# Performance work log

Hardware: AMD Instinct MI355X
Metric: run time of the kernel (lower is better)

Reference implementation:

```python
import jax, jax.numpy as jnp
import numpy as np

B, H, W, C = 16, 56, 56, 512
HEADS, WIN = 16, 7
HID = 2048
EPS = 1e-5


def _rel_pos_index(win):
    coords = np.stack(np.meshgrid(np.arange(win), np.arange(win), indexing='ij'))  # 2,w,w
    cf = coords.reshape(2, -1)  # 2, w*w
    rel = (cf[:, :, None] - cf[:, None, :]).transpose(1, 2, 0).astype(np.int64)  # N,N,2
    rel[..., 0] += win - 1
    rel[..., 1] += win - 1
    rel[..., 0] *= 2 * win - 1
    return jnp.asarray(rel.sum(-1))  # N,N


def setup_inputs() -> dict:
    key = jax.random.key(0)
    ks = jax.random.split(key, 12)
    s = 0.02
    return {
        'x': jax.random.normal(ks[0], (B, H * W, C), jnp.float32),
        'norm1_w': jnp.ones((C,), jnp.float32),
        'norm1_b': jnp.zeros((C,), jnp.float32),
        'qkv_w': jax.random.normal(ks[1], (3 * C, C), jnp.float32) * s,
        'qkv_b': jnp.zeros((3 * C,), jnp.float32),
        'proj_w': jax.random.normal(ks[2], (C, C), jnp.float32) * s,
        'proj_b': jnp.zeros((C,), jnp.float32),
        'rel_bias_table': jax.random.normal(ks[3], ((2 * WIN - 1) ** 2, HEADS), jnp.float32) * s,
        'norm2_w': jnp.ones((C,), jnp.float32),
        'norm2_b': jnp.zeros((C,), jnp.float32),
        'fc1_w': jax.random.normal(ks[4], (HID, C), jnp.float32) * s,
        'fc1_b': jnp.zeros((HID,), jnp.float32),
        'fc2_w': jax.random.normal(ks[5], (C, HID), jnp.float32) * s,
        'fc2_b': jnp.zeros((C,), jnp.float32),
        'rel_pos_index': _rel_pos_index(WIN),
    }


def _ln(x, w, b):
    m = jnp.mean(x, -1, keepdims=True)
    v = jnp.mean((x - m) ** 2, -1, keepdims=True)
    return (x - m) * jax.lax.rsqrt(v + EPS) * w + b


def reference(x, norm1_w, norm1_b, qkv_w, qkv_b, proj_w, proj_b, rel_bias_table,
              norm2_w, norm2_b, fc1_w, fc1_b, fc2_w, fc2_b, rel_pos_index):
    N = WIN * WIN
    hd = C // HEADS
    shortcut = x
    h = _ln(x, norm1_w, norm1_b).reshape(B, H, W, C)
    # window partition -> (nW*B, N, C)
    h = h.reshape(B, H // WIN, WIN, W // WIN, WIN, C).transpose(0, 1, 3, 2, 4, 5)
    xw = h.reshape(-1, N, C)
    Bw = xw.shape[0]
    qkv = (xw @ qkv_w.T + qkv_b).reshape(Bw, N, 3, HEADS, hd).transpose(2, 0, 3, 1, 4)
    q, k, v = qkv[0], qkv[1], qkv[2]  # (Bw, heads, N, hd)
    q = q * (hd ** -0.5)
    attn = jnp.einsum('bhnd,bhmd->bhnm', q, k)
    bias = rel_bias_table[rel_pos_index.reshape(-1)].reshape(N, N, HEADS).transpose(2, 0, 1)
    attn = jax.nn.softmax(attn + bias[None], axis=-1)
    out = jnp.einsum('bhnm,bhmd->bhnd', attn, v).transpose(0, 2, 1, 3).reshape(Bw, N, C)
    out = out @ proj_w.T + proj_b
    # window reverse -> (B, H*W, C)
    out = out.reshape(B, H // WIN, W // WIN, WIN, WIN, C).transpose(0, 1, 3, 2, 4, 5)
    out = out.reshape(B, H * W, C)
    x = shortcut + out
    h2 = _ln(x, norm2_w, norm2_b)
    h2 = jax.nn.gelu(h2 @ fc1_w.T + fc1_b, approximate=False) @ fc2_w.T + fc2_b
    return x + h2
```

## Files before the change

kernel.cpp:

```cpp
#include <hip/hip_runtime.h>
#include <stdint.h>

#define B_    16
#define C_    512
#define HEADS 16
#define NTOK  49
#define ROWS  (16*56*56)

typedef __attribute__((ext_vector_type(8))) __bf16 bf16x8;
typedef __attribute__((ext_vector_type(4))) float  f32x4;
typedef __attribute__((ext_vector_type(8))) unsigned short u16x8;
typedef __attribute__((ext_vector_type(4))) unsigned short u16x4;

__device__ __forceinline__ unsigned short f2bf(float f) {
  union { float f; uint32_t u; } x; x.f = f;
  uint32_t r = x.u + 0x7FFFu + ((x.u >> 16) & 1u);
  return (unsigned short)(r >> 16);
}
__device__ __forceinline__ float bf2f(unsigned short u) {
  union { uint32_t u; float f; } x; x.u = ((uint32_t)u) << 16;
  return x.f;
}

template<int EPI>
__global__ __launch_bounds__(512, 2)
void gemm_bt(const unsigned short* __restrict__ A,
             const unsigned short* __restrict__ Bt,
             const float* __restrict__ bias,
             const float* __restrict__ res,
             void* __restrict__ outp,
             int N, int K, int ldb, int nbn)
{
  __shared__ __align__(16) unsigned short As[2][256*64];
  __shared__ __align__(16) unsigned short Bs[2][256*64];

  const int nwg = gridDim.x;
  const int q8 = nwg >> 3, r8 = nwg & 7;
  const int xcd = blockIdx.x & 7, ixc = blockIdx.x >> 3;
  const int l = (xcd < r8 ? xcd * (q8 + 1) : r8 * (q8 + 1) + (xcd - r8) * q8) + ixc;
  const int bm = l / nbn, bn = l % nbn;

  const int tid  = threadIdx.x;
  const int wave = tid >> 6;
  const int lane = tid & 63;
  const int wr = wave >> 2, wc = wave & 3;

  const unsigned short* Ag = A  + (size_t)bm * 256 * K;
  const unsigned short* Bg = Bt + (size_t)bn * 256 * ldb;

  f32x4 acc[8][4] = {};
  const int fr = lane & 15;
  const int kq = lane >> 4;
  const int sx = fr & 7;

  auto STAGE = [&](int buf, int t) {
    const int k0 = t << 6;
    #pragma unroll
    for (int li = 0; li < 4; ++li) {
      const int slot = tid + li * 512;
      const int r = slot >> 3;
      const int g = (slot & 7) ^ (r & 7);
      __builtin_amdgcn_global_load_lds(
        (const __attribute__((address_space(1))) void*)(Ag + (size_t)r * K + k0 + g * 8),
        (__attribute__((address_space(3))) void*)(&As[buf][(li * 512 + wave * 64) * 8]), 16, 0, 0);
    }
    #pragma unroll
    for (int li = 0; li < 4; ++li) {
      const int slot = tid + li * 512;
      const int r = slot >> 3;
      const int g = (slot & 7) ^ (r & 7);
      __builtin_amdgcn_global_load_lds(
        (const __attribute__((address_space(1))) void*)(Bg + (size_t)r * ldb + k0 + g * 8),
        (__attribute__((address_space(3))) void*)(&Bs[buf][(li * 512 + wave * 64) * 8]), 16, 0, 0);
    }
  };

  const int nt = K >> 6;
  STAGE(0, 0);
  for (int t = 0; t < nt; ++t) {
    const int c = t & 1;
    if (t + 1 < nt) {
      STAGE(c ^ 1, t + 1);
      asm volatile("s_waitcnt vmcnt(8)" ::: "memory");
    } else {
      asm volatile("s_waitcnt vmcnt(0)" ::: "memory");
    }
    __builtin_amdgcn_s_barrier();

    #pragma unroll
    for (int ks = 0; ks < 2; ++ks) {
      bf16x8 a[8], b[4];
      #pragma unroll
      for (int m = 0; m < 8; ++m)
        a[m] = *(const bf16x8*)&As[c][(wr * 128 + m * 16 + fr) * 64
                                      + (((ks * 4 + kq) ^ sx) * 8)];
      #pragma unroll
      for (int n = 0; n < 4; ++n)
        b[n] = *(const bf16x8*)&Bs[c][(wc * 64 + n * 16 + fr) * 64
                                      + (((ks * 4 + kq) ^ sx) * 8)];
      __builtin_amdgcn_s_setprio(1);
      #pragma unroll
      for (int m = 0; m < 8; ++m)
        #pragma unroll
        for (int n = 0; n < 4; ++n)
          acc[m][n] = __builtin_amdgcn_mfma_f32_16x16x32_bf16(a[m], b[n], acc[m][n], 0, 0, 0);
      __builtin_amdgcn_s_setprio(0);
    }

    asm volatile("s_waitcnt lgkmcnt(0)" ::: "memory");
    __builtin_amdgcn_s_barrier();
  }

  const int rq = lane >> 4;
  #pragma unroll
  for (int m = 0; m < 8; ++m) {
    #pragma unroll
    for (int n = 0; n < 4; ++n) {
      const int gcol = bn * 256 + wc * 64 + n * 16 + fr;
      const float bv = (EPI == 3) ? 0.f : bias[gcol];
      #pragma unroll
      for (int r = 0; r < 4; ++r) {
        const int grow = bm * 256 + wr * 128 + m * 16 + rq * 4 + r;
        const size_t off = (size_t)grow * N + gcol;
        float v = acc[m][n][r] + bv;
        if (EPI == 0) {
          ((unsigned short*)outp)[off] = f2bf(v);
        } else if (EPI == 1) {
          v = 0.5f * v * (1.0f + erff(v * 0.70710678118654752f));
          ((unsigned short*)outp)[off] = f2bf(v);
        } else {
          ((float*)outp)[off] = v + res[off];
        }
      }
    }
  }
}

__global__ __launch_bounds__(256)
void ln_bf16(const float* __restrict__ x, const float* __restrict__ w,
             const float* __restrict__ b, unsigned short* __restrict__ out)
{
  const int row  = blockIdx.x * 4 + (threadIdx.x >> 6);
  const int lane = threadIdx.x & 63;
  const float4* xr = (const float4*)(x + (size_t)row * C_);
  const float4 u = xr[lane * 2];
  const float4 v = xr[lane * 2 + 1];
  const float vals[8] = {u.x,u.y,u.z,u.w,v.x,v.y,v.z,v.w};
  float s = 0.f, s2 = 0.f;
  #pragma unroll
  for (int j = 0; j < 8; ++j) { s += vals[j]; s2 += vals[j]*vals[j]; }
  #pragma unroll
  for (int off = 1; off < 64; off <<= 1) {
    s  += __shfl_xor(s,  off);
    s2 += __shfl_xor(s2, off);
  }
  const float mean = s * (1.0f/512.0f);
  const float rstd = rsqrtf(s2 * (1.0f/512.0f) - mean*mean + 1e-5f);
  u16x8 o;
  #pragma unroll
  for (int j = 0; j < 8; ++j) {
    const int col = lane * 8 + j;
    o[j] = f2bf((vals[j] - mean) * rstd * w[col] + b[col]);
  }
  *(u16x8*)&out[(size_t)row * C_ + lane * 8] = o;
}

__global__ __launch_bounds__(512)
void attn_win2(const unsigned short* __restrict__ qkv,
               const unsigned short* __restrict__ biasBf,
               unsigned short* __restrict__ outb, int i0)
{
  __shared__ float  Ksh[8][NTOK*32];
  __shared__ float  Vsh[8][NTOK*32];
  __shared__ unsigned short Bsh[8][NTOK*NTOK];
  const int bi   = blockIdx.x;
  const int half = bi & 1, winl = bi >> 1;
  const int bbl = winl >> 6, wy = (winl >> 3) & 7, wx = winl & 7;
  const int wave = threadIdx.x >> 6, lane = threadIdx.x & 63;
  const int head = half * 8 + wave;

  for (int i = lane; i < NTOK*NTOK; i += 64)
    Bsh[wave][i] = biasBf[head * (NTOK*NTOK) + i];

  float q[32];
  size_t gl = 0, gg = 0;
  if (lane < NTOK) {
    const int r = lane / 7, c = lane % 7;
    gl = (size_t)bbl * 3136 + (size_t)((wy*7 + r) * 56 + (wx*7 + c));
    gg = gl + (size_t)i0 * 3136;
    const unsigned short* qp = qkv + gl * 1536 + head * 32;
    #pragma unroll
    for (int d = 0; d < 32; d += 4) {
      const u16x4 qv = *(const u16x4*)&qp[d];
      const u16x4 kv = *(const u16x4*)&qp[512 + d];
      const u16x4 vv = *(const u16x4*)&qp[1024 + d];
      #pragma unroll
      for (int e = 0; e < 4; ++e) {
        q[d+e] = bf2f(qv[e]);
        Ksh[wave][lane*32 + d + e] = bf2f(kv[e]);
        Vsh[wave][lane*32 + d + e] = bf2f(vv[e]);
      }
    }
  }
  if (lane < NTOK) {
    float s[NTOK];
    float mx = -1e30f;
    for (int j = 0; j < NTOK; ++j) {
      float dot = 0.f;
      #pragma unroll
      for (int d = 0; d < 32; ++d) dot += q[d] * Ksh[wave][j*32 + d];
      const float val = dot * 0.17677669529663687f
                      + bf2f(Bsh[wave][lane*NTOK + j]);
      s[j] = val;
      mx = fmaxf(mx, val);
    }
    float sum = 0.f;
    for (int j = 0; j < NTOK; ++j) { s[j] = __expf(s[j] - mx); sum += s[j]; }
    const float inv = 1.0f / sum;
    float o[32];
    #pragma unroll
    for (int d = 0; d < 32; ++d) o[d] = 0.f;
    for (int j = 0; j < NTOK; ++j) {
      const float p = s[j] * inv;
      #pragma unroll
      for (int d = 0; d < 32; ++d) o[d] += p * Vsh[wave][j*32 + d];
    }
    unsigned short* op = outb + gg * 512 + head * 32;
    #pragma unroll
    for (int d = 0; d < 32; d += 4) {
      u16x4 ov;
      #pragma unroll
      for (int e = 0; e < 4; ++e) ov[e] = f2bf(o[d+e]);
      *(u16x4*)&op[d] = ov;
    }
  }
}

__global__ void build_bias(const float* __restrict__ table, const int* __restrict__ idx,
                           unsigned short* __restrict__ biasBf)
{
  const int i = blockIdx.x * 256 + threadIdx.x;
  if (i >= HEADS * NTOK * NTOK) return;
  const int h  = i / (NTOK*NTOK);
  const int ij = i - h * (NTOK*NTOK);
  biasBf[i] = f2bf(table[idx[ij] * HEADS + h]);
}

__global__ void conv_bf16(const float* __restrict__ in, unsigned short* __restrict__ out, int n4)
{
  const int i = blockIdx.x * 256 + threadIdx.x;
  if (i >= n4) return;
  const float4 v = ((const float4*)in)[i];
  u16x4 o; o[0]=f2bf(v.x); o[1]=f2bf(v.y); o[2]=f2bf(v.z); o[3]=f2bf(v.w);
  ((u16x4*)out)[i] = o;
}

extern "C" void kernel_launch(void* const* d_in, const int* in_sizes, int n_in,
                              void* d_out, int out_size, void* d_ws, size_t ws_size,
                              hipStream_t stream)
{
  const float* x     = (const float*)d_in[0];
  const float* n1w   = (const float*)d_in[1];
  const float* n1b   = (const float*)d_in[2];
  const float* qkvw  = (const float*)d_in[3];
  const float* qkvb  = (const float*)d_in[4];
  const float* projw = (const float*)d_in[5];
  const float* projb = (const float*)d_in[6];
  const float* rbt   = (const float*)d_in[7];
  const float* n2w   = (const float*)d_in[8];
  const float* n2b   = (const float*)d_in[9];
  const float* fc1w  = (const float*)d_in[10];
  const float* fc1b  = (const float*)d_in[11];
  const float* fc2w  = (const float*)d_in[12];
  const float* fc2b  = (const float*)d_in[13];
  const int*   rpi   = (const int*)d_in[14];
  float* out = (float*)d_out;

  char* p = (char*)d_ws;
  auto alloc = [&](size_t bytes) -> char* {
    char* q = p; p += (bytes + 255) & ~(size_t)255; return q;
  };
  unsigned short* wqB  = (unsigned short*)alloc((size_t)1536 * 512 * 2);
  unsigned short* wpB  = (unsigned short*)alloc((size_t)512  * 512 * 2);
  unsigned short* w1B  = (unsigned short*)alloc((size_t)2048 * 512 * 2);
  unsigned short* w2B  = (unsigned short*)alloc((size_t)512  * 2048 * 2);
  unsigned short* biasBf = (unsigned short*)alloc((size_t)HEADS * NTOK * NTOK * 2);
  unsigned short* bufX = (unsigned short*)alloc((size_t)ROWS * 512 * 2);
  const size_t used = (size_t)(p - (char*)d_ws);
  const size_t Rbytes = (ws_size > used) ? ws_size - used : 0;
  unsigned short* R = (unsigned short*)p;

  int ic = 0;
  for (int c = 16; c >= 4; c >>= 1)
    if ((size_t)c * 3136 * 1536 * 2 <= Rbytes) { ic = c; break; }
  int hc = 0;
  for (int c = 2048; c >= 256; c >>= 1)
    if ((size_t)ROWS * c * 2 <= Rbytes) { hc = c; break; }
  if (ic == 0 || hc == 0) return;

  conv_bf16<<<(1536*512/4 + 255)/256, 256, 0, stream>>>(qkvw, wqB, 1536*512/4);
  conv_bf16<<<(512*512/4  + 255)/256, 256, 0, stream>>>(projw, wpB, 512*512/4);
  conv_bf16<<<(2048*512/4 + 255)/256, 256, 0, stream>>>(fc1w, w1B, 2048*512/4);
  conv_bf16<<<(512*2048/4 + 255)/256, 256, 0, stream>>>(fc2w, w2B, 512*2048/4);
  build_bias<<<(HEADS*NTOK*NTOK + 255)/256, 256, 0, stream>>>(rbt, rpi, biasBf);

  ln_bf16<<<ROWS/4, 256, 0, stream>>>(x, n1w, n1b, bufX);

  for (int i0 = 0; i0 < B_; i0 += ic) {
    const int nbm = ic * 3136 / 256, nbn = 6;
    gemm_bt<0><<<nbm * nbn, 512, 0, stream>>>(
        bufX + (size_t)i0*3136*512, wqB, qkvb, nullptr, R, 1536, 512, 512, nbn);
    attn_win2<<<ic*64*2, 512, 0, stream>>>(R, biasBf, bufX, i0);
  }

  gemm_bt<2><<<(ROWS/256) * 2, 512, 0, stream>>>(
      bufX, wpB, projb, x, out, 512, 512, 512, 2);

  ln_bf16<<<ROWS/4, 256, 0, stream>>>(out, n2w, n2b, bufX);

  for (int h0 = 0; h0 < 2048; h0 += hc) {
    gemm_bt<1><<<(ROWS/256) * (hc/256), 512, 0, stream>>>(
        bufX, w1B + (size_t)h0*512, fc1b + h0, nullptr, R, hc, 512, 512, hc/256);
    if (h0 == 0)
      gemm_bt<2><<<(ROWS/256) * 2, 512, 0, stream>>>(
          R, w2B + h0, fc2b, out, out, 512, hc, 2048, 2);
    else
      gemm_bt<3><<<(ROWS/256) * 2, 512, 0, stream>>>(
          R, w2B + h0, nullptr, out, out, 512, hc, 2048, 2);
  }
}
```

Measured before the change: 861.4 us.

## Use 4-stage 32-wide K pipeline in GEMM and tanh-approx GELU

Restructures the GEMM main loop from a double-buffered BK=64 scheme into a four-deep ring of BK=32 stages, with three stages of loads in flight and an adjusted LDS swizzle. The goal is to hide more global memory latency behind MFMA work with the same LDS footprint, at the cost of a barrier pair per 32-wide K step. It also replaces the exact erf GELU with a tanh-form approximation built on a sigmoid and fast exp. That is cheaper per element but departs from the reference's exact GELU (approximate=False).

```diff
diff --git a/kernel.cpp b/kernel.cpp
--- a/kernel.cpp
+++ b/kernel.cpp
@@ -11,6 +11,9 @@
 typedef __attribute__((ext_vector_type(4))) float  f32x4;
 typedef __attribute__((ext_vector_type(8))) unsigned short u16x8;
 typedef __attribute__((ext_vector_type(4))) unsigned short u16x4;
+
+#define AS1 __attribute__((address_space(1)))
+#define AS3 __attribute__((address_space(3)))
 
 __device__ __forceinline__ unsigned short f2bf(float f) {
   union { float f; uint32_t u; } x; x.f = f;
@@ -31,8 +34,8 @@
              void* __restrict__ outp,
              int N, int K, int ldb, int nbn)
 {
-  __shared__ __align__(16) unsigned short As[2][256*64];
-  __shared__ __align__(16) unsigned short Bs[2][256*64];
+  __shared__ __align__(16) unsigned short As[4 * 8192];
+  __shared__ __align__(16) unsigned short Bs[4 * 8192];
 
   const int nwg = gridDim.x;
   const int q8 = nwg >> 3, r8 = nwg & 7;
@@ -51,64 +54,67 @@
   f32x4 acc[8][4] = {};
   const int fr = lane & 15;
   const int kq = lane >> 4;
-  const int sx = fr & 7;
-
-  auto STAGE = [&](int buf, int t) {
-    const int k0 = t << 6;
-    #pragma unroll
-    for (int li = 0; li < 4; ++li) {
-      const int slot = tid + li * 512;
-      const int r = slot >> 3;
-      const int g = (slot & 7) ^ (r & 7);
+  const int kxor = kq ^ (fr & 3);
+
+  auto STAGE = [&](int s) {
+    const int r = s & 3;
+    const int k0 = s << 5;
+    #pragma unroll
+    for (int i = 0; i < 2; ++i) {
+      const int u = tid + i * 512;
+      const int row = u >> 2;
+      const int gs = (u & 3) ^ (row & 3);
       __builtin_amdgcn_global_load_lds(
-        (const __attribute__((address_space(1))) void*)(Ag + (size_t)r * K + k0 + g * 8),
-        (__attribute__((address_space(3))) void*)(&As[buf][(li * 512 + wave * 64) * 8]), 16, 0, 0);
-    }
-    #pragma unroll
-    for (int li = 0; li < 4; ++li) {
-      const int slot = tid + li * 512;
-      const int r = slot >> 3;
-      const int g = (slot & 7) ^ (r & 7);
+        (const AS1 void*)(Ag + (size_t)row * K + k0 + gs * 8),
+        (AS3 void*)(&As[r * 8192 + (wave * 64 + i * 512) * 8]), 16, 0, 0);
+    }
+    #pragma unroll
+    for (int i = 0; i < 2; ++i) {
+      const int u = tid + i * 512;
+      const int row = u >> 2;
+      const int gs = (u & 3) ^ (row & 3);
       __builtin_amdgcn_global_load_lds(
-        (const __attribute__((address_space(1))) void*)(Bg + (size_t)r * ldb + k0 + g * 8),
-        (__attribute__((address_space(3))) void*)(&Bs[buf][(li * 512 + wave * 64) * 8]), 16, 0, 0);
+        (const AS1 void*)(Bg + (size_t)row * ldb + k0 + gs * 8),
+        (AS3 void*)(&Bs[r * 8192 + (wave * 64 + i * 512) * 8]), 16, 0, 0);
     }
   };
 
-  const int nt = K >> 6;
-  STAGE(0, 0);
-  for (int t = 0; t < nt; ++t) {
-    const int c = t & 1;
-    if (t + 1 < nt) {
-      STAGE(c ^ 1, t + 1);
-      asm volatile("s_waitcnt vmcnt(8)" ::: "memory");
-    } else {
-      asm volatile("s_waitcnt vmcnt(0)" ::: "memory");
-    }
+  const int NS = K >> 5;
+  STAGE(0);
+  if (NS > 1) STAGE(1);
+  if (NS > 2) STAGE(2);
+
+  for (int s = 0; s < NS; ++s) {
+    if (s + 3 < NS) STAGE(s + 3);
+
+    const int rem = NS - 1 - s;
+    if (rem >= 3)      asm volatile("s_waitcnt vmcnt(12)" ::: "memory");
+    else if (rem == 2) asm volatile("s_waitcnt vmcnt(8)"  ::: "memory");
+    else if (rem == 1) asm volatile("s_waitcnt vmcnt(4)"  ::: "memory");
+    else               asm volatile("s_waitcnt vmcnt(0)"  ::: "memory");
     __builtin_amdgcn_s_barrier();
-
-    #pragma unroll
-    for (int ks = 0; ks < 2; ++ks) {
-      bf16x8 a[8], b[4];
-      #pragma unroll
-      for (int m = 0; m < 8; ++m)
-        a[m] = *(const bf16x8*)&As[c][(wr * 128 + m * 16 + fr) * 64
-                                      + (((ks * 4 + kq) ^ sx) * 8)];
+    asm volatile("" ::: "memory");
+
+    const int r = s & 3;
+    bf16x8 a[8], b[4];
+    #pragma unroll
+    for (int m = 0; m < 8; ++m)
+      a[m] = *(const bf16x8*)&As[r * 8192 + (wr * 128 + m * 16 + fr) * 32 + kxor * 8];
+    #pragma unroll
+    for (int n = 0; n < 4; ++n)
+      b[n] = *(const bf16x8*)&Bs[r * 8192 + (wc * 64 + n * 16 + fr) * 32 + kxor * 8];
+
+    __builtin_amdgcn_s_setprio(1);
+    #pragma unroll
+    for (int m = 0; m < 8; ++m)
       #pragma unroll
       for (int n = 0; n < 4; ++n)
-        b[n] = *(const bf16x8*)&Bs[c][(wc * 64 + n * 16 + fr) * 64
-                                      + (((ks * 4 + kq) ^ sx) * 8)];
-      __builtin_amdgcn_s_setprio(1);
-      #pragma unroll
-      for (int m = 0; m < 8; ++m)
-        #pragma unroll
-        for (int n = 0; n < 4; ++n)
-          acc[m][n] = __builtin_amdgcn_mfma_f32_16x16x32_bf16(a[m], b[n], acc[m][n], 0, 0, 0);
-      __builtin_amdgcn_s_setprio(0);
-    }
+        acc[m][n] = __builtin_amdgcn_mfma_f32_16x16x32_bf16(a[m], b[n], acc[m][n], 0, 0, 0);
+    __builtin_amdgcn_s_setprio(0);
 
     asm volatile("s_waitcnt lgkmcnt(0)" ::: "memory");
     __builtin_amdgcn_s_barrier();
+    asm volatile("" ::: "memory");
   }
 
   const int rq = lane >> 4;
@@ -126,7 +132,8 @@
         if (EPI == 0) {
           ((unsigned short*)outp)[off] = f2bf(v);
         } else if (EPI == 1) {
-          v = 0.5f * v * (1.0f + erff(v * 0.70710678118654752f));
+          const float u2 = 1.5957691216f * v * (1.0f + 0.044715f * v * v);
+          v = v / (1.0f + __expf(-u2));
           ((unsigned short*)outp)[off] = f2bf(v);
         } else {
           ((float*)outp)[off] = v + res[off];
```

Measured after the change: 926.3 us. 1.08x slower.
